# Kernel optimization log

Hardware: AMD Instinct MI355X
Metric: run time of the kernel (lower is better)

Reference implementation:

```python
import jax, jax.numpy as jnp
import numpy as np

IN_F = 128
OUT_F = 128
N_LAYER = 2
DEPTH = 9                       # tree depth -> levels 0..DEPTH-1
N_TREES = 128
TREE_SIZE = 2 ** DEPTH - 1      # 511 nodes per complete binary tree
N = N_TREES * TREE_SIZE         # 65408 total nodes
E = N_TREES * (TREE_SIZE - 1)   # 65280 parent->child edges


def _build_forest():
    """Complete binary trees in heap layout; leaves get order 0, root order DEPTH-1."""
    k = np.arange(TREE_SIZE)
    depth = np.floor(np.log2(k + 1)).astype(np.int32)
    order_tree = (DEPTH - 1) - depth                      # per-node level within a tree
    node_order = np.tile(order_tree, N_TREES).astype(np.int32)
    internal = k[k < 2 ** (DEPTH - 1) - 1]                # internal nodes have 2 children
    par = np.repeat(internal, 2)
    chi = np.empty_like(par)
    chi[0::2] = 2 * internal + 1
    chi[1::2] = 2 * internal + 2
    eorder_tree = order_tree[par]
    offs = (np.arange(N_TREES) * TREE_SIZE)[:, None]
    parents = (par[None, :] + offs).reshape(-1)
    children = (chi[None, :] + offs).reshape(-1)
    adjacency = np.stack([parents, children], axis=1).astype(np.int32)
    edge_order = np.tile(eorder_tree, N_TREES).astype(np.int32)
    return node_order, adjacency, edge_order


def setup_inputs() -> dict:
    key = jax.random.key(0)
    ks = jax.random.split(key, 8)
    node_order, adjacency, edge_order = _build_forest()
    s = 0.05
    return {
        "features": jax.random.normal(ks[0], (N, IN_F), jnp.float32),
        "W_iou": jax.random.normal(ks[1], (N_LAYER, 3 * OUT_F, IN_F), jnp.float32) * s,
        "b_iou": jax.random.normal(ks[2], (N_LAYER, 3 * OUT_F), jnp.float32) * s,
        "U_iou": jax.random.normal(ks[3], (N_LAYER, 3 * OUT_F, OUT_F), jnp.float32) * s,
        "W_f": jax.random.normal(ks[4], (N_LAYER, OUT_F, IN_F), jnp.float32) * s,
        "b_f": jax.random.normal(ks[5], (N_LAYER, OUT_F), jnp.float32) * s,
        "U_f": jax.random.normal(ks[6], (N_LAYER, OUT_F, OUT_F), jnp.float32) * s,
        "node_order": jnp.asarray(node_order),
        "adjacency_list": jnp.asarray(adjacency),
        "edge_order": jnp.asarray(edge_order),
        "treesizes": jnp.full((N_TREES,), TREE_SIZE, jnp.int32),
        "n_levels": DEPTH,
    }


def reference(features, W_iou, b_iou, U_iou, W_f, b_f, U_f,
              node_order, adjacency_list, edge_order, treesizes, n_levels):
    n_nodes = features.shape[0]
    parent = adjacency_list[:, 0]
    child = adjacency_list[:, 1]
    n_trees = treesizes.shape[0]
    tree_size = n_nodes // n_trees
    # root of each (equal-sized) tree = argmax of node_order within its segment
    root_idx = (jnp.argmax(node_order.reshape(n_trees, tree_size), axis=1)
                + jnp.arange(n_trees) * tree_size)

    def run_layer(Wi, bi, Ui, Wf, bf, Uf):
        Wx_iou = features @ Wi.T + bi              # [N, 3H], level-independent
        Wfx = features[parent] @ Wf.T + bf         # [E, H], per-edge forget input
        H = Wi.shape[0] // 3

        def step(carry, lvl):
            h, c = carry
            em = (edge_order == lvl).astype(features.dtype)[:, None]   # [E,1]
            ch = h[child]                                              # gather child h
            cc = c[child]
            h_sum = jax.ops.segment_sum(ch * em, parent, num_segments=n_nodes)
            iou = Wx_iou + h_sum @ Ui.T
            i_, o_, u_ = jnp.split(iou, 3, axis=1)
            i_ = jax.nn.sigmoid(i_)
            o_ = jax.nn.sigmoid(o_)
            u_ = jnp.tanh(u_)
            f = jax.nn.sigmoid(Wfx + ch @ Uf.T)                        # [E,H]
            c_sum = jax.ops.segment_sum(f * cc * em, parent, num_segments=n_nodes)
            c_new = i_ * u_ + c_sum
            h_new = o_ * jnp.tanh(c_new)
            nm = (node_order == lvl)[:, None]
            return (jnp.where(nm, h_new, h), jnp.where(nm, c_new, c)), None

        init = (jnp.zeros((n_nodes, H), features.dtype),
                jnp.zeros((n_nodes, H), features.dtype))
        (h, c), _ = jax.lax.scan(step, init, jnp.arange(n_levels))
        return h[root_idx], c[root_idx]

    f_h, f_c = jax.vmap(run_layer)(W_iou, b_iou, U_iou, W_f, b_f, U_f)
    return f_h, f_c
```

## Files before the change

### kernel.cpp

```cpp
#include <hip/hip_runtime.h>
#include <hip/hip_bf16.h>


#define TS 511
#define NT 128
#define NN (NT * TS)

typedef __attribute__((ext_vector_type(8))) short short8;
typedef __attribute__((ext_vector_type(4))) float floatx4;

#define MFMA_B16 __builtin_amdgcn_mfma_f32_16x16x32_bf16

#define BARLDS() do { \
    asm volatile("s_waitcnt lgkmcnt(0)" ::: "memory"); \
    __builtin_amdgcn_s_barrier(); \
    asm volatile("" ::: "memory"); \
} while (0)

__device__ __forceinline__ unsigned short f2b(float f) {
    return __builtin_bit_cast(unsigned short, __float2bfloat16(f));
}
__device__ __forceinline__ float b2f_u(unsigned short u) {
    unsigned v = (unsigned)u << 16;
    return __builtin_bit_cast(float, v);
}
__device__ __forceinline__ float rcp_(float x) { return __builtin_amdgcn_rcpf(x); }
__device__ __forceinline__ float sig_(float x) { return rcp_(1.0f + __expf(-x)); }
__device__ __forceinline__ float tanh_(float x) {
    float a = fabsf(x);
    float t = __expf(-2.0f * a);
    return copysignf((1.0f - t) * rcp_(1.0f + t), x);
}

__global__ void pack_b(const float* __restrict__ Wiou, const float* __restrict__ biou,
                       const float* __restrict__ Uiou, const float* __restrict__ Wf,
                       const float* __restrict__ bfv, const float* __restrict__ Uf,
                       const float* __restrict__ feat,
                       unsigned short* __restrict__ BgU, unsigned short* __restrict__ BgX,
                       float* __restrict__ bp5, unsigned short* __restrict__ xb) {
    int tid = blockIdx.x * 256 + threadIdx.x;
    if (tid < 1280) {
        int l = tid / 640, r = tid % 640, g = r >> 7, o = r & 127;
        bp5[tid] = (g < 3) ? biou[l * 384 + r] : bfv[l * 128 + o];
    }
    if (tid < 131072) {
        int l = tid >> 16, r = tid & 65535, col = r >> 7, kp = r & 127;
        float v = (col < 384) ? Uiou[(l * 384 + col) * 128 + kp]
                              : Uf[(l * 128 + (col - 384)) * 128 + kp];
        BgU[((size_t)(l * 512 + col)) * 128 + kp] = f2b(v);
    } else if (tid < 262144) {
        int e2 = tid - 131072;
        int l = e2 >> 16, r = e2 & 65535, col = r >> 7, kp = r & 127;
        float v = (col < 384) ? Wiou[(l * 384 + col) * 128 + kp]
                              : Wf[(l * 128 + (col - 384)) * 128 + kp];
        BgX[((size_t)(l * 512 + col)) * 128 + kp] = f2b(v);
    } else {
        int e = tid - 262144;
        size_t base = (size_t)e * 8;
        float4 v0 = *(const float4*)(feat + base);
        float4 v1 = *(const float4*)(feat + base + 4);
        short8 r;
        r[0] = (short)f2b(v0.x); r[1] = (short)f2b(v0.y);
        r[2] = (short)f2b(v0.z); r[3] = (short)f2b(v0.w);
        r[4] = (short)f2b(v1.x); r[5] = (short)f2b(v1.y);
        r[6] = (short)f2b(v1.z); r[7] = (short)f2b(v1.w);
        *(short8*)(xb + base) = r;
    }
}

__global__ __launch_bounds__(512, 2) void forest(
        const unsigned short* __restrict__ xb16, const unsigned short* __restrict__ BgU,
        const unsigned short* __restrict__ BgX, const float* __restrict__ bp5,
        float* __restrict__ out) {
    __shared__ __align__(16) unsigned short S[69632];
    const int HC0 = 26112;

    const int tid = threadIdx.x;
    const int l = blockIdx.x >> 7, tree = blockIdx.x & 127;
    const int lane = tid & 63, w = tid >> 6;
    const int quad = lane >> 4, l15 = lane & 15;
    const int o = w * 16 + l15;
    const unsigned short* xb = xb16 + (size_t)tree * TS * 128;
    const unsigned short* BU = BgU + (size_t)l * 512 * 128;
    const unsigned short* BX = BgX + (size_t)l * 512 * 128;

    short8 bU[4][4], bX[4][4];
#pragma unroll
    for (int g = 0; g < 4; g++) {
        const size_t cb = (size_t)(g * 128 + o) * 128;
#pragma unroll
        for (int kbl = 0; kbl < 4; kbl++) {
            bU[g][kbl] = *(const short8*)(BU + cb + kbl * 32 + quad * 8);
            bX[g][kbl] = *(const short8*)(BX + cb + kbl * 32 + quad * 8);
        }
    }
    float bb[5];
#pragma unroll
    for (int g = 0; g < 5; g++) bb[g] = bp5[l * 640 + g * 128 + o];

    auto ldx = [&](int heap, int kbl) -> short8 {
        return *(const short8*)(xb + (size_t)heap * 128 + kbl * 32 + quad * 8);
    };

    auto ltile = [&](int heapA, int selfH, int selfC) {
        floatx4 ai = (floatx4){0.f, 0.f, 0.f, 0.f};
        floatx4 ao = ai, au = ai;
#pragma unroll
        for (int kbl = 0; kbl < 4; kbl++) {
            short8 ax = ldx(heapA, kbl);
            ai = MFMA_B16(ax, bX[0][kbl], ai, 0, 0, 0);
            ao = MFMA_B16(ax, bX[1][kbl], ao, 0, 0, 0);
            au = MFMA_B16(ax, bX[2][kbl], au, 0, 0, 0);
        }
#pragma unroll
        for (int r = 0; r < 4; r++) {
            int idx = quad * 4 + r;
            float iv = sig_(ai[r] + bb[0]);
            float ov = sig_(ao[r] + bb[1]);
            float uv = tanh_(au[r] + bb[2]);
            float cn = iv * uv;
            float hn = ov * tanh_(cn);
            S[(selfH + idx) * 136 + o] = f2b(hn);
            S[HC0 + (selfC + idx) * 136 + o] = f2b(cn);
        }
    };

    auto itile = [&](int heapA, int chAh, int selfRB, int chRBc,
                     int nValid, bool isRoot) {
        floatx4 ai = (floatx4){0.f, 0.f, 0.f, 0.f};
        floatx4 ao = ai, au = ai, awx = ai, af0 = ai, af1 = ai;
#pragma unroll
        for (int kbl = 0; kbl < 4; kbl++) {
            short8 h0 = *(const short8*)&S[chAh * 136 + kbl * 32 + quad * 8];
            short8 h1 = *(const short8*)&S[(chAh + 1) * 136 + kbl * 32 + quad * 8];
            short8 ax = ldx(heapA, kbl);
            ai = MFMA_B16(h0, bU[0][kbl], ai, 0, 0, 0);
            ai = MFMA_B16(h1, bU[0][kbl], ai, 0, 0, 0);
            ao = MFMA_B16(h0, bU[1][kbl], ao, 0, 0, 0);
            ao = MFMA_B16(h1, bU[1][kbl], ao, 0, 0, 0);
            au = MFMA_B16(h0, bU[2][kbl], au, 0, 0, 0);
            au = MFMA_B16(h1, bU[2][kbl], au, 0, 0, 0);
            af0 = MFMA_B16(h0, bU[3][kbl], af0, 0, 0, 0);
            af1 = MFMA_B16(h1, bU[3][kbl], af1, 0, 0, 0);
            ai = MFMA_B16(ax, bX[0][kbl], ai, 0, 0, 0);
            ao = MFMA_B16(ax, bX[1][kbl], ao, 0, 0, 0);
            au = MFMA_B16(ax, bX[2][kbl], au, 0, 0, 0);
            awx = MFMA_B16(ax, bX[3][kbl], awx, 0, 0, 0);
        }
#pragma unroll
        for (int r = 0; r < 4; r++) {
            int idx = quad * 4 + r;
            if (idx < nValid) {
                float iv = sig_(ai[r] + bb[0]);
                float ov = sig_(ao[r] + bb[1]);
                float uv = tanh_(au[r] + bb[2]);
                float f0 = sig_(awx[r] + af0[r] + bb[3]);
                float f1 = sig_(awx[r] + af1[r] + bb[4]);
                float c0 = b2f_u(S[HC0 + (chRBc + 2 * idx) * 136 + o]);
                float c1 = b2f_u(S[HC0 + (chRBc + 2 * idx + 1) * 136 + o]);
                float cn = iv * uv + f0 * c0 + f1 * c1;
                float hn = ov * tanh_(cn);
                S[(selfRB + idx) * 136 + o] = f2b(hn);
                S[HC0 + (selfRB + idx) * 136 + o] = f2b(cn);
                if (isRoot) {
                    out[((size_t)l * 128 + tree) * 128 + o] = hn;
                    out[32768 + ((size_t)l * 128 + tree) * 128 + o] = cn;
                }
            }
        }
    };

#pragma unroll
    for (int s = 0; s < 2; s++)
        ltile(255 + s * 16 + l15, 384 + s * 16, 256 + s * 16);
    BARLDS();

#pragma unroll 2
    for (int t = 0; t < 8; t++) {
        if (t < 7) {
            int b2 = (t + 1) & 1;
#pragma unroll
            for (int s = 0; s < 2; s++)
                ltile(255 + (t + 1) * 32 + s * 16 + l15,
                      384 + b2 * 32 + s * 16, 256 + b2 * 32 + s * 16);
        }
        int b = t & 1;
        itile(127 + t * 16 + l15,
              384 + b * 32 + 2 * l15,
              t * 16,
              256 + b * 32,
              16, false);
        BARLDS();
    }

#pragma unroll
    for (int dd = 6; dd >= 0; dd--) {
        const int nd = 1 << dd;
        const int selfB = (dd == 6) ? 128 : 64 - 2 * nd;
        const int chB = (dd == 6) ? 0 : ((dd == 5) ? 128 : 64 - 4 * nd);
        const int mts = (nd + 15) >> 4;
#pragma unroll
        for (int mt = 0; mt < mts; mt++) {
            int rl = mt * 16 + l15;
            if (rl > nd - 1) rl = nd - 1;
            int nv = nd - mt * 16;
            if (nv > 16) nv = 16;
            itile(nd - 1 + rl,
                  chB + 2 * rl,
                  selfB + mt * 16,
                  chB + 2 * mt * 16,
                  nv, dd == 0);
        }
        BARLDS();
    }
}

extern "C" void kernel_launch(void* const* d_in, const int* in_sizes, int n_in,
                              void* d_out, int out_size, void* d_ws, size_t ws_size,
                              hipStream_t stream) {
    const float* feat = (const float*)d_in[0];
    const float* Wiou = (const float*)d_in[1];
    const float* biou = (const float*)d_in[2];
    const float* Uiou = (const float*)d_in[3];
    const float* Wf   = (const float*)d_in[4];
    const float* bfv  = (const float*)d_in[5];
    const float* Uf   = (const float*)d_in[6];
    float* out = (float*)d_out;

    unsigned short* BgU = (unsigned short*)d_ws;
    unsigned short* BgX = BgU + (size_t)131072;
    unsigned short* xb16 = BgX + (size_t)131072;
    float* bp5 = (float*)(xb16 + (size_t)NN * 128);

    pack_b<<<5112, 256, 0, stream>>>(Wiou, biou, Uiou, Wf, bfv, Uf, feat,
                                     BgU, BgX, bp5, xb16);
    forest<<<256, 512, 0, stream>>>(xb16, BgU, BgX, bp5, out);
}
```

Before: 157.6 us.

## Prefetch feature tiles ahead of MFMA and interleave upper tree levels into leaf loop

Global loads of bf16 feature rows are hoisted into whole-tile prefetches issued before the MFMA work that consumes them, so memory latency overlaps compute instead of being exposed inside the k-loop. Level-6 internal tiles are folded into the main level-7/8 loop on alternate iterations, and the remaining upper levels are unrolled by hand with next-level features prefetched before each barrier. The goal is fewer barriers and less exposed load latency. The cost is higher register pressure from holding several X4 prefetch buffers, and the hand-coded LDS row offsets must match the old layout exactly.

```diff
diff --git a/kernel.cpp b/kernel.cpp
--- a/kernel.cpp
+++ b/kernel.cpp
@@ -101,16 +101,22 @@
     auto ldx = [&](int heap, int kbl) -> short8 {
         return *(const short8*)(xb + (size_t)heap * 128 + kbl * 32 + quad * 8);
     };
-
-    auto ltile = [&](int heapA, int selfH, int selfC) {
+    struct X4 { short8 a[4]; };
+    auto pfx = [&](int heap) -> X4 {
+        X4 r;
+#pragma unroll
+        for (int k = 0; k < 4; k++) r.a[k] = ldx(heap, k);
+        return r;
+    };
+
+    auto ltile = [&](const X4& ax, int selfH, int selfC) {
         floatx4 ai = (floatx4){0.f, 0.f, 0.f, 0.f};
         floatx4 ao = ai, au = ai;
 #pragma unroll
         for (int kbl = 0; kbl < 4; kbl++) {
-            short8 ax = ldx(heapA, kbl);
-            ai = MFMA_B16(ax, bX[0][kbl], ai, 0, 0, 0);
-            ao = MFMA_B16(ax, bX[1][kbl], ao, 0, 0, 0);
-            au = MFMA_B16(ax, bX[2][kbl], au, 0, 0, 0);
+            ai = MFMA_B16(ax.a[kbl], bX[0][kbl], ai, 0, 0, 0);
+            ao = MFMA_B16(ax.a[kbl], bX[1][kbl], ao, 0, 0, 0);
+            au = MFMA_B16(ax.a[kbl], bX[2][kbl], au, 0, 0, 0);
         }
 #pragma unroll
         for (int r = 0; r < 4; r++) {
@@ -125,7 +131,7 @@
         }
     };
 
-    auto itile = [&](int heapA, int chAh, int selfRB, int chRBc,
+    auto itile = [&](const X4& ax, int chAh, int selfRB, int chRBc,
                      int nValid, bool isRoot) {
         floatx4 ai = (floatx4){0.f, 0.f, 0.f, 0.f};
         floatx4 ao = ai, au = ai, awx = ai, af0 = ai, af1 = ai;
@@ -133,7 +139,6 @@
         for (int kbl = 0; kbl < 4; kbl++) {
             short8 h0 = *(const short8*)&S[chAh * 136 + kbl * 32 + quad * 8];
             short8 h1 = *(const short8*)&S[(chAh + 1) * 136 + kbl * 32 + quad * 8];
-            short8 ax = ldx(heapA, kbl);
             ai = MFMA_B16(h0, bU[0][kbl], ai, 0, 0, 0);
             ai = MFMA_B16(h1, bU[0][kbl], ai, 0, 0, 0);
             ao = MFMA_B16(h0, bU[1][kbl], ao, 0, 0, 0);
@@ -142,10 +147,10 @@
             au = MFMA_B16(h1, bU[2][kbl], au, 0, 0, 0);
             af0 = MFMA_B16(h0, bU[3][kbl], af0, 0, 0, 0);
             af1 = MFMA_B16(h1, bU[3][kbl], af1, 0, 0, 0);
-            ai = MFMA_B16(ax, bX[0][kbl], ai, 0, 0, 0);
-            ao = MFMA_B16(ax, bX[1][kbl], ao, 0, 0, 0);
-            au = MFMA_B16(ax, bX[2][kbl], au, 0, 0, 0);
-            awx = MFMA_B16(ax, bX[3][kbl], awx, 0, 0, 0);
+            ai = MFMA_B16(ax.a[kbl], bX[0][kbl], ai, 0, 0, 0);
+            ao = MFMA_B16(ax.a[kbl], bX[1][kbl], ao, 0, 0, 0);
+            au = MFMA_B16(ax.a[kbl], bX[2][kbl], au, 0, 0, 0);
+            awx = MFMA_B16(ax.a[kbl], bX[3][kbl], awx, 0, 0, 0);
         }
 #pragma unroll
         for (int r = 0; r < 4; r++) {
@@ -170,49 +175,55 @@
         }
     };
 
-#pragma unroll
-    for (int s = 0; s < 2; s++)
-        ltile(255 + s * 16 + l15, 384 + s * 16, 256 + s * 16);
-    BARLDS();
-
-#pragma unroll 2
+    {
+        X4 p0 = pfx(255 + l15), p1 = pfx(271 + l15);
+        ltile(p0, 384, 256);
+        ltile(p1, 400, 272);
+    }
+    BARLDS();
+
+    X4 axT0, axT1;
+
+#pragma unroll 1
     for (int t = 0; t < 8; t++) {
+        X4 lx0, lx1, axd, axe;
+        axd = pfx(127 + t * 16 + l15);
+        if (t < 7) { lx0 = pfx(287 + t * 32 + l15); lx1 = pfx(303 + t * 32 + l15); }
+        const bool do6 = (t == 2) || (t == 4) || (t == 6);
+        const int j = (t - 2) >> 1;
+        if (do6) axe = pfx(63 + j * 16 + l15);
+        if (t == 7) { axT0 = pfx(111 + l15); axT1 = pfx(31 + l15); }
+
+        const int b = t & 1, b2 = b ^ 1;
         if (t < 7) {
-            int b2 = (t + 1) & 1;
-#pragma unroll
-            for (int s = 0; s < 2; s++)
-                ltile(255 + (t + 1) * 32 + s * 16 + l15,
-                      384 + b2 * 32 + s * 16, 256 + b2 * 32 + s * 16);
-        }
-        int b = t & 1;
-        itile(127 + t * 16 + l15,
-              384 + b * 32 + 2 * l15,
-              t * 16,
-              256 + b * 32,
-              16, false);
+            ltile(lx0, 384 + b2 * 32, 256 + b2 * 32);
+            ltile(lx1, 384 + b2 * 32 + 16, 256 + b2 * 32 + 16);
+        }
+        itile(axd, 384 + b * 32 + 2 * l15, t * 16, 256 + b * 32, 16, false);
+        if (do6) itile(axe, 2 * (j * 16 + l15), 128 + j * 16, 32 * j, 16, false);
         BARLDS();
     }
 
-#pragma unroll
-    for (int dd = 6; dd >= 0; dd--) {
-        const int nd = 1 << dd;
-        const int selfB = (dd == 6) ? 128 : 64 - 2 * nd;
-        const int chB = (dd == 6) ? 0 : ((dd == 5) ? 128 : 64 - 4 * nd);
-        const int mts = (nd + 15) >> 4;
-#pragma unroll
-        for (int mt = 0; mt < mts; mt++) {
-            int rl = mt * 16 + l15;
-            if (rl > nd - 1) rl = nd - 1;
-            int nv = nd - mt * 16;
-            if (nv > 16) nv = 16;
-            itile(nd - 1 + rl,
-                  chB + 2 * rl,
-                  selfB + mt * 16,
-                  chB + 2 * mt * 16,
-                  nv, dd == 0);
-        }
-        BARLDS();
-    }
+    itile(axT0, 96 + 2 * l15, 176, 96, 16, false);
+    itile(axT1, 128 + 2 * l15, 0, 128, 16, false);
+    axT0 = pfx(47 + l15);
+    BARLDS();
+    itile(axT0, 160 + 2 * l15, 16, 160, 16, false);
+    axT0 = pfx(15 + l15);
+    BARLDS();
+    itile(axT0, 2 * l15, 32, 0, 16, false);
+    { int rl = (l15 < 7) ? l15 : 7; axT0 = pfx(7 + rl); }
+    BARLDS();
+    { int rl = (l15 < 7) ? l15 : 7; itile(axT0, 32 + 2 * rl, 48, 32, 8, false); }
+    { int rl = (l15 < 3) ? l15 : 3; axT0 = pfx(3 + rl); }
+    BARLDS();
+    { int rl = (l15 < 3) ? l15 : 3; itile(axT0, 48 + 2 * rl, 56, 48, 4, false); }
+    { int rl = (l15 < 1) ? l15 : 1; axT0 = pfx(1 + rl); }
+    BARLDS();
+    { int rl = (l15 < 1) ? l15 : 1; itile(axT0, 56 + 2 * rl, 60, 56, 2, false); }
+    axT0 = pfx(0);
+    BARLDS();
+    itile(axT0, 60, 62, 60, 1, true);
 }
 
 extern "C" void kernel_launch(void* const* d_in, const int* in_sizes, int n_in,
```

Result: slower. 170.6 us (+8.2%).

## Prefetch node features into registers and interleave level-6 tiles with level-7 loop

Applied to the files above, without the earlier changes.

Global loads of the bf16 node features are now issued one stage ahead into registers instead of being read inside the MFMA loops, which hides their global-memory latency behind the previous tile's compute. Level-6 internal tiles are folded into the level-7 loop as soon as their children are ready, which removes separate barrier phases, and the upper levels are unrolled by hand with explicit prefetches. Launch bounds change to waves_per_eu(2,2). The extra live short8 registers raise register pressure and could cause spills.

```diff
diff --git a/kernel.cpp b/kernel.cpp
--- a/kernel.cpp
+++ b/kernel.cpp
@@ -68,7 +68,9 @@
     }
 }
 
-__global__ __launch_bounds__(512, 2) void forest(
+__global__ __launch_bounds__(512, 1)
+__attribute__((amdgpu_waves_per_eu(2, 2)))
+void forest(
         const unsigned short* __restrict__ xb16, const unsigned short* __restrict__ BgU,
         const unsigned short* __restrict__ BgX, const float* __restrict__ bp5,
         float* __restrict__ out) {
@@ -102,12 +104,13 @@
         return *(const short8*)(xb + (size_t)heap * 128 + kbl * 32 + quad * 8);
     };
 
-    auto ltile = [&](int heapA, int selfH, int selfC) {
+    auto ltile = [&](short8 a0, short8 a1, short8 a2, short8 a3,
+                     int selfH, int selfC) {
         floatx4 ai = (floatx4){0.f, 0.f, 0.f, 0.f};
         floatx4 ao = ai, au = ai;
 #pragma unroll
         for (int kbl = 0; kbl < 4; kbl++) {
-            short8 ax = ldx(heapA, kbl);
+            short8 ax = (kbl == 0) ? a0 : (kbl == 1) ? a1 : (kbl == 2) ? a2 : a3;
             ai = MFMA_B16(ax, bX[0][kbl], ai, 0, 0, 0);
             ao = MFMA_B16(ax, bX[1][kbl], ao, 0, 0, 0);
             au = MFMA_B16(ax, bX[2][kbl], au, 0, 0, 0);
@@ -125,15 +128,15 @@
         }
     };
 
-    auto itile = [&](int heapA, int chAh, int selfRB, int chRBc,
-                     int nValid, bool isRoot) {
+    auto itile = [&](short8 a0, short8 a1, short8 a2, short8 a3,
+                     int chAh, int selfRB, int chRBc, int nValid, bool isRoot) {
         floatx4 ai = (floatx4){0.f, 0.f, 0.f, 0.f};
         floatx4 ao = ai, au = ai, awx = ai, af0 = ai, af1 = ai;
 #pragma unroll
         for (int kbl = 0; kbl < 4; kbl++) {
+            short8 ax = (kbl == 0) ? a0 : (kbl == 1) ? a1 : (kbl == 2) ? a2 : a3;
             short8 h0 = *(const short8*)&S[chAh * 136 + kbl * 32 + quad * 8];
             short8 h1 = *(const short8*)&S[(chAh + 1) * 136 + kbl * 32 + quad * 8];
-            short8 ax = ldx(heapA, kbl);
             ai = MFMA_B16(h0, bU[0][kbl], ai, 0, 0, 0);
             ai = MFMA_B16(h1, bU[0][kbl], ai, 0, 0, 0);
             ao = MFMA_B16(h0, bU[1][kbl], ao, 0, 0, 0);
@@ -170,49 +173,96 @@
         }
     };
 
-#pragma unroll
-    for (int s = 0; s < 2; s++)
-        ltile(255 + s * 16 + l15, 384 + s * 16, 256 + s * 16);
-    BARLDS();
-
-#pragma unroll 2
+    short8 axdC[4];
+    short8 axT0[4], axT1[4];
+
+    {
+        short8 t0[4], t1[4];
+#pragma unroll
+        for (int k = 0; k < 4; k++) {
+            t0[k] = ldx(255 + l15, k);
+            t1[k] = ldx(271 + l15, k);
+            axdC[k] = ldx(127 + l15, k);
+        }
+        ltile(t0[0], t0[1], t0[2], t0[3], 384, 256);
+        ltile(t1[0], t1[1], t1[2], t1[3], 400, 272);
+    }
+    BARLDS();
+
+#pragma unroll 1
     for (int t = 0; t < 8; t++) {
+        const int b = t & 1;
+        const bool do6 = (t >= 2) && !(t & 1);
+        const int j = (t - 2) >> 1;
+        short8 lx0[4], lx1[4], axe[4];
         if (t < 7) {
-            int b2 = (t + 1) & 1;
-#pragma unroll
-            for (int s = 0; s < 2; s++)
-                ltile(255 + (t + 1) * 32 + s * 16 + l15,
-                      384 + b2 * 32 + s * 16, 256 + b2 * 32 + s * 16);
-        }
-        int b = t & 1;
-        itile(127 + t * 16 + l15,
-              384 + b * 32 + 2 * l15,
-              t * 16,
-              256 + b * 32,
-              16, false);
+#pragma unroll
+            for (int k = 0; k < 4; k++) {
+                lx0[k] = ldx(287 + t * 32 + l15, k);
+                lx1[k] = ldx(303 + t * 32 + l15, k);
+            }
+        }
+        if (do6) {
+#pragma unroll
+            for (int k = 0; k < 4; k++) axe[k] = ldx(63 + j * 16 + l15, k);
+        }
+        if (t == 7) {
+#pragma unroll
+            for (int k = 0; k < 4; k++) {
+                axT0[k] = ldx(111 + l15, k);
+                axT1[k] = ldx(31 + l15, k);
+            }
+        }
+
+        itile(axdC[0], axdC[1], axdC[2], axdC[3],
+              384 + b * 32 + 2 * l15, t * 16, 256 + b * 32, 16, false);
+        if (t < 7) {
+#pragma unroll
+            for (int k = 0; k < 4; k++) axdC[k] = ldx(127 + (t + 1) * 16 + l15, k);
+        }
+        if (do6)
+            itile(axe[0], axe[1], axe[2], axe[3],
+                  2 * (j * 16 + l15), 128 + j * 16, 32 * j, 16, false);
+        if (t < 7) {
+            const int b2 = b ^ 1;
+            ltile(lx0[0], lx0[1], lx0[2], lx0[3], 384 + b2 * 32, 256 + b2 * 32);
+            ltile(lx1[0], lx1[1], lx1[2], lx1[3], 384 + b2 * 32 + 16, 256 + b2 * 32 + 16);
+        }
         BARLDS();
     }
 
-#pragma unroll
-    for (int dd = 6; dd >= 0; dd--) {
-        const int nd = 1 << dd;
-        const int selfB = (dd == 6) ? 128 : 64 - 2 * nd;
-        const int chB = (dd == 6) ? 0 : ((dd == 5) ? 128 : 64 - 4 * nd);
-        const int mts = (nd + 15) >> 4;
-#pragma unroll
-        for (int mt = 0; mt < mts; mt++) {
-            int rl = mt * 16 + l15;
-            if (rl > nd - 1) rl = nd - 1;
-            int nv = nd - mt * 16;
-            if (nv > 16) nv = 16;
-            itile(nd - 1 + rl,
-                  chB + 2 * rl,
-                  selfB + mt * 16,
-                  chB + 2 * mt * 16,
-                  nv, dd == 0);
-        }
-        BARLDS();
-    }
+    itile(axT0[0], axT0[1], axT0[2], axT0[3], 96 + 2 * l15, 176, 96, 16, false);
+    itile(axT1[0], axT1[1], axT1[2], axT1[3], 128 + 2 * l15, 0, 128, 16, false);
+#pragma unroll
+    for (int k = 0; k < 4; k++) axT0[k] = ldx(47 + l15, k);
+    BARLDS();
+    itile(axT0[0], axT0[1], axT0[2], axT0[3], 160 + 2 * l15, 16, 160, 16, false);
+#pragma unroll
+    for (int k = 0; k < 4; k++) axT0[k] = ldx(15 + l15, k);
+    BARLDS();
+    itile(axT0[0], axT0[1], axT0[2], axT0[3], 2 * l15, 32, 0, 16, false);
+    { int rl = (l15 < 7) ? l15 : 7;
+#pragma unroll
+      for (int k = 0; k < 4; k++) axT0[k] = ldx(7 + rl, k); }
+    BARLDS();
+    { int rl = (l15 < 7) ? l15 : 7;
+      itile(axT0[0], axT0[1], axT0[2], axT0[3], 32 + 2 * rl, 48, 32, 8, false); }
+    { int rl = (l15 < 3) ? l15 : 3;
+#pragma unroll
+      for (int k = 0; k < 4; k++) axT0[k] = ldx(3 + rl, k); }
+    BARLDS();
+    { int rl = (l15 < 3) ? l15 : 3;
+      itile(axT0[0], axT0[1], axT0[2], axT0[3], 48 + 2 * rl, 56, 48, 4, false); }
+    { int rl = (l15 < 1) ? l15 : 1;
+#pragma unroll
+      for (int k = 0; k < 4; k++) axT0[k] = ldx(1 + rl, k); }
+    BARLDS();
+    { int rl = (l15 < 1) ? l15 : 1;
+      itile(axT0[0], axT0[1], axT0[2], axT0[3], 56 + 2 * rl, 60, 56, 2, false); }
+#pragma unroll
+    for (int k = 0; k < 4; k++) axT0[k] = ldx(0, k);
+    BARLDS();
+    itile(axT0[0], axT0[1], axT0[2], axT0[3], 60, 62, 60, 1, true);
 }
 
 extern "C" void kernel_launch(void* const* d_in, const int* in_sizes, int n_in,
```

Result: slower. 180.0 us (+14.2%).

## Split leaf-level LSTM into a separate wide GEMM kernel before tree recursion

Applied to the files above, without the earlier changes.

Leaf node computation (x·W_iou, gates) moves out of the per-tree forest kernel into a new leafwx kernel. It runs as a batched MFMA GEMM across all trees and both layers and writes leaf h/c in bf16 to global memory. The forest kernel now reads leaf h/c from global, packs features only for internal nodes, and loads U/W fragments from global per use instead of keeping them in registers. The aim is to parallelise the dominant leaf work across many more blocks and to lower register pressure in the recursive kernel. In exchange it adds a kernel launch, an extra global round trip for leaf states, and repeated weight loads in the inner loops.

```diff
diff --git a/kernel.cpp b/kernel.cpp
--- a/kernel.cpp
+++ b/kernel.cpp
@@ -4,7 +4,6 @@
 
 #define TS 511
 #define NT 128
-#define NN (NT * TS)
 
 typedef __attribute__((ext_vector_type(8))) short short8;
 typedef __attribute__((ext_vector_type(4))) float floatx4;
@@ -56,112 +55,210 @@
         BgX[((size_t)(l * 512 + col)) * 128 + kp] = f2b(v);
     } else {
         int e = tid - 262144;
-        size_t base = (size_t)e * 8;
-        float4 v0 = *(const float4*)(feat + base);
-        float4 v1 = *(const float4*)(feat + base + 4);
+        int tree = e / 4080;
+        int rem = e - tree * 4080;
+        int row = rem >> 4, c8 = (rem & 15) * 8;
+        const float* src = feat + ((size_t)tree * TS + row) * 128 + c8;
+        float4 v0 = *(const float4*)src;
+        float4 v1 = *(const float4*)(src + 4);
         short8 r;
         r[0] = (short)f2b(v0.x); r[1] = (short)f2b(v0.y);
         r[2] = (short)f2b(v0.z); r[3] = (short)f2b(v0.w);
         r[4] = (short)f2b(v1.x); r[5] = (short)f2b(v1.y);
         r[6] = (short)f2b(v1.z); r[7] = (short)f2b(v1.w);
-        *(short8*)(xb + base) = r;
+        *(short8*)(xb + ((size_t)tree * 255 + row) * 128 + c8) = r;
     }
 }
 
-__global__ __launch_bounds__(512, 2) void forest(
-        const unsigned short* __restrict__ xb16, const unsigned short* __restrict__ BgU,
+__global__ __launch_bounds__(256) void leafwx(
+        const float* __restrict__ feat, const unsigned short* __restrict__ BgX,
+        const float* __restrict__ bp5,
+        unsigned short* __restrict__ hb, unsigned short* __restrict__ cb) {
+    const int tid = threadIdx.x;
+    const int lane = tid & 63, wave = tid >> 6;
+    const int W = blockIdx.x * 4 + wave;
+    const int wn = W & 3;
+    const int mt = W >> 2;
+    const int l = mt >> 10, m = mt & 1023;
+    const int quad = lane >> 4, l15 = lane & 15;
+    const unsigned short* BX = BgX + (size_t)l * 512 * 128;
+
+    floatx4 acc[2][6];
+#pragma unroll
+    for (int mi = 0; mi < 2; mi++)
+#pragma unroll
+        for (int ni = 0; ni < 6; ni++)
+            acc[mi][ni] = (floatx4){0.f, 0.f, 0.f, 0.f};
+
+#pragma unroll
+    for (int kb = 0; kb < 4; kb++) {
+        short8 bfr[6];
+#pragma unroll
+        for (int ni = 0; ni < 6; ni++) {
+            int col = (ni >> 1) * 128 + wn * 32 + (ni & 1) * 16 + l15;
+            bfr[ni] = *(const short8*)(BX + (size_t)col * 128 + kb * 32 + quad * 8);
+        }
+#pragma unroll
+        for (int mi = 0; mi < 2; mi++) {
+            int j = m * 32 + mi * 16 + l15;
+            int tree = j >> 8, li = j & 255;
+            const float* p = feat + ((size_t)tree * TS + 255 + li) * 128 + kb * 32 + quad * 8;
+            float4 u0 = *(const float4*)p;
+            float4 u1 = *(const float4*)(p + 4);
+            short8 a;
+            a[0] = (short)f2b(u0.x); a[1] = (short)f2b(u0.y);
+            a[2] = (short)f2b(u0.z); a[3] = (short)f2b(u0.w);
+            a[4] = (short)f2b(u1.x); a[5] = (short)f2b(u1.y);
+            a[6] = (short)f2b(u1.z); a[7] = (short)f2b(u1.w);
+#pragma unroll
+            for (int ni = 0; ni < 6; ni++)
+                acc[mi][ni] = MFMA_B16(a, bfr[ni], acc[mi][ni], 0, 0, 0);
+        }
+    }
+#pragma unroll
+    for (int mi = 0; mi < 2; mi++)
+#pragma unroll
+        for (int ch = 0; ch < 2; ch++) {
+            int of = wn * 32 + ch * 16 + l15;
+            float bi = bp5[l * 640 + of];
+            float bo = bp5[l * 640 + 128 + of];
+            float bu = bp5[l * 640 + 256 + of];
+#pragma unroll
+            for (int r = 0; r < 4; r++) {
+                int j = m * 32 + mi * 16 + quad * 4 + r;
+                int tree = j >> 8, li = j & 255;
+                float iv = sig_(acc[mi][ch][r] + bi);
+                float ov = sig_(acc[mi][2 + ch][r] + bo);
+                float uv = tanh_(acc[mi][4 + ch][r] + bu);
+                float cn = iv * uv;
+                float hn = ov * tanh_(cn);
+                size_t idx = ((size_t)(l * 32768) + tree * 256 + li) * 128 + of;
+                hb[idx] = f2b(hn);
+                cb[idx] = f2b(cn);
+            }
+        }
+}
+
+__global__ __launch_bounds__(512) void forest(
+        const unsigned short* __restrict__ xb16, const unsigned short* __restrict__ hbL,
+        const unsigned short* __restrict__ cbL, const unsigned short* __restrict__ BgU,
         const unsigned short* __restrict__ BgX, const float* __restrict__ bp5,
         float* __restrict__ out) {
-    __shared__ __align__(16) unsigned short S[69632];
-    const int HC0 = 26112;
+    __shared__ __align__(16) unsigned short S[69360];
+    const int HC0 = 34680;
 
     const int tid = threadIdx.x;
     const int l = blockIdx.x >> 7, tree = blockIdx.x & 127;
     const int lane = tid & 63, w = tid >> 6;
     const int quad = lane >> 4, l15 = lane & 15;
     const int o = w * 16 + l15;
-    const unsigned short* xb = xb16 + (size_t)tree * TS * 128;
+    const unsigned short* xb = xb16 + (size_t)tree * 255 * 128;
+    const unsigned short* lh = hbL + ((size_t)(l * 32768) + tree * 256) * 128;
+    const unsigned short* lc = cbL + ((size_t)(l * 32768) + tree * 256) * 128;
     const unsigned short* BU = BgU + (size_t)l * 512 * 128;
     const unsigned short* BX = BgX + (size_t)l * 512 * 128;
 
-    short8 bU[4][4], bX[4][4];
-#pragma unroll
-    for (int g = 0; g < 4; g++) {
-        const size_t cb = (size_t)(g * 128 + o) * 128;
-#pragma unroll
-        for (int kbl = 0; kbl < 4; kbl++) {
-            bU[g][kbl] = *(const short8*)(BU + cb + kbl * 32 + quad * 8);
-            bX[g][kbl] = *(const short8*)(BX + cb + kbl * 32 + quad * 8);
-        }
-    }
     float bb[5];
 #pragma unroll
     for (int g = 0; g < 5; g++) bb[g] = bp5[l * 640 + g * 128 + o];
 
-    auto ldx = [&](int heap, int kbl) -> short8 {
-        return *(const short8*)(xb + (size_t)heap * 128 + kbl * 32 + quad * 8);
-    };
-
-    auto ltile = [&](int heapA, int selfH, int selfC) {
+    auto bu_ = [&](int g, int k) -> short8 {
+        return *(const short8*)(BU + ((size_t)(g * 128 + o)) * 128 + k * 32 + quad * 8);
+    };
+    auto bx_ = [&](int g, int k) -> short8 {
+        return *(const short8*)(BX + ((size_t)(g * 128 + o)) * 128 + k * 32 + quad * 8);
+    };
+    auto ldx = [&](int heap, int k) -> short8 {
+        return *(const short8*)(xb + (size_t)heap * 128 + k * 32 + quad * 8);
+    };
+
+    auto itile_g = [&](int t) {
+        const int nA = 127 + t * 16 + l15;
+        const int li0 = 32 * t + 2 * l15;
+        short8 ax[4];
+#pragma unroll
+        for (int k = 0; k < 4; k++) ax[k] = ldx(nA, k);
         floatx4 ai = (floatx4){0.f, 0.f, 0.f, 0.f};
-        floatx4 ao = ai, au = ai;
-#pragma unroll
-        for (int kbl = 0; kbl < 4; kbl++) {
-            short8 ax = ldx(heapA, kbl);
-            ai = MFMA_B16(ax, bX[0][kbl], ai, 0, 0, 0);
-            ao = MFMA_B16(ax, bX[1][kbl], ao, 0, 0, 0);
-            au = MFMA_B16(ax, bX[2][kbl], au, 0, 0, 0);
+        floatx4 ao = ai, au = ai, awx = ai, af0 = ai, af1 = ai;
+#pragma unroll
+        for (int k = 0; k < 4; k++) {
+            short8 h0 = *(const short8*)(lh + (size_t)li0 * 128 + k * 32 + quad * 8);
+            short8 h1 = *(const short8*)(lh + (size_t)(li0 + 1) * 128 + k * 32 + quad * 8);
+            ai = MFMA_B16(h0, bu_(0, k), ai, 0, 0, 0);
+            ai = MFMA_B16(h1, bu_(0, k), ai, 0, 0, 0);
+            ao = MFMA_B16(h0, bu_(1, k), ao, 0, 0, 0);
+            ao = MFMA_B16(h1, bu_(1, k), ao, 0, 0, 0);
+            au = MFMA_B16(h0, bu_(2, k), au, 0, 0, 0);
+            au = MFMA_B16(h1, bu_(2, k), au, 0, 0, 0);
+            af0 = MFMA_B16(h0, bu_(3, k), af0, 0, 0, 0);
+            af1 = MFMA_B16(h1, bu_(3, k), af1, 0, 0, 0);
+            ai = MFMA_B16(ax[k], bx_(0, k), ai, 0, 0, 0);
+            ao = MFMA_B16(ax[k], bx_(1, k), ao, 0, 0, 0);
+            au = MFMA_B16(ax[k], bx_(2, k), au, 0, 0, 0);
+            awx = MFMA_B16(ax[k], bx_(3, k), awx, 0, 0, 0);
         }
 #pragma unroll
         for (int r = 0; r < 4; r++) {
             int idx = quad * 4 + r;
+            int node = 127 + t * 16 + idx;
+            int lic = 32 * t + 2 * idx;
             float iv = sig_(ai[r] + bb[0]);
             float ov = sig_(ao[r] + bb[1]);
             float uv = tanh_(au[r] + bb[2]);
-            float cn = iv * uv;
+            float f0 = sig_(awx[r] + af0[r] + bb[3]);
+            float f1 = sig_(awx[r] + af1[r] + bb[4]);
+            float c0 = b2f_u(lc[(size_t)lic * 128 + o]);
+            float c1 = b2f_u(lc[(size_t)(lic + 1) * 128 + o]);
+            float cn = iv * uv + f0 * c0 + f1 * c1;
             float hn = ov * tanh_(cn);
-            S[(selfH + idx) * 136 + o] = f2b(hn);
-            S[HC0 + (selfC + idx) * 136 + o] = f2b(cn);
-        }
-    };
-
-    auto itile = [&](int heapA, int chAh, int selfRB, int chRBc,
-                     int nValid, bool isRoot) {
+            S[node * 136 + o] = f2b(hn);
+            S[HC0 + node * 136 + o] = f2b(cn);
+        }
+    };
+
+    auto itile_l = [&](int base, int nv, bool isRoot) {
+        const int rl = (l15 < nv) ? l15 : nv - 1;
+        const int nA = base + rl;
+        const int ch0 = 2 * nA + 1;
+        short8 ax[4];
+#pragma unroll
+        for (int k = 0; k < 4; k++) ax[k] = ldx(nA, k);
         floatx4 ai = (floatx4){0.f, 0.f, 0.f, 0.f};
         floatx4 ao = ai, au = ai, awx = ai, af0 = ai, af1 = ai;
 #pragma unroll
-        for (int kbl = 0; kbl < 4; kbl++) {
-            short8 h0 = *(const short8*)&S[chAh * 136 + kbl * 32 + quad * 8];
-            short8 h1 = *(const short8*)&S[(chAh + 1) * 136 + kbl * 32 + quad * 8];
-            short8 ax = ldx(heapA, kbl);
-            ai = MFMA_B16(h0, bU[0][kbl], ai, 0, 0, 0);
-            ai = MFMA_B16(h1, bU[0][kbl], ai, 0, 0, 0);
-            ao = MFMA_B16(h0, bU[1][kbl], ao, 0, 0, 0);
-            ao = MFMA_B16(h1, bU[1][kbl], ao, 0, 0, 0);
-            au = MFMA_B16(h0, bU[2][kbl], au, 0, 0, 0);
-            au = MFMA_B16(h1, bU[2][kbl], au, 0, 0, 0);
-            af0 = MFMA_B16(h0, bU[3][kbl], af0, 0, 0, 0);
-            af1 = MFMA_B16(h1, bU[3][kbl], af1, 0, 0, 0);
-            ai = MFMA_B16(ax, bX[0][kbl], ai, 0, 0, 0);
-            ao = MFMA_B16(ax, bX[1][kbl], ao, 0, 0, 0);
-            au = MFMA_B16(ax, bX[2][kbl], au, 0, 0, 0);
-            awx = MFMA_B16(ax, bX[3][kbl], awx, 0, 0, 0);
+        for (int k = 0; k < 4; k++) {
+            short8 h0 = *(const short8*)&S[ch0 * 136 + k * 32 + quad * 8];
+            short8 h1 = *(const short8*)&S[(ch0 + 1) * 136 + k * 32 + quad * 8];
+            ai = MFMA_B16(h0, bu_(0, k), ai, 0, 0, 0);
+            ai = MFMA_B16(h1, bu_(0, k), ai, 0, 0, 0);
+            ao = MFMA_B16(h0, bu_(1, k), ao, 0, 0, 0);
+            ao = MFMA_B16(h1, bu_(1, k), ao, 0, 0, 0);
+            au = MFMA_B16(h0, bu_(2, k), au, 0, 0, 0);
+            au = MFMA_B16(h1, bu_(2, k), au, 0, 0, 0);
+            af0 = MFMA_B16(h0, bu_(3, k), af0, 0, 0, 0);
+            af1 = MFMA_B16(h1, bu_(3, k), af1, 0, 0, 0);
+            ai = MFMA_B16(ax[k], bx_(0, k), ai, 0, 0, 0);
+            ao = MFMA_B16(ax[k], bx_(1, k), ao, 0, 0, 0);
+            au = MFMA_B16(ax[k], bx_(2, k), au, 0, 0, 0);
+            awx = MFMA_B16(ax[k], bx_(3, k), awx, 0, 0, 0);
         }
 #pragma unroll
         for (int r = 0; r < 4; r++) {
             int idx = quad * 4 + r;
-            if (idx < nValid) {
+            if (idx < nv) {
+                int node = base + idx;
+                int ch = 2 * node + 1;
                 float iv = sig_(ai[r] + bb[0]);
                 float ov = sig_(ao[r] + bb[1]);
                 float uv = tanh_(au[r] + bb[2]);
                 float f0 = sig_(awx[r] + af0[r] + bb[3]);
                 float f1 = sig_(awx[r] + af1[r] + bb[4]);
-                float c0 = b2f_u(S[HC0 + (chRBc + 2 * idx) * 136 + o]);
-                float c1 = b2f_u(S[HC0 + (chRBc + 2 * idx + 1) * 136 + o]);
+                float c0 = b2f_u(S[HC0 + ch * 136 + o]);
+                float c1 = b2f_u(S[HC0 + (ch + 1) * 136 + o]);
                 float cn = iv * uv + f0 * c0 + f1 * c1;
                 float hn = ov * tanh_(cn);
-                S[(selfRB + idx) * 136 + o] = f2b(hn);
-                S[HC0 + (selfRB + idx) * 136 + o] = f2b(cn);
+                S[node * 136 + o] = f2b(hn);
+                S[HC0 + node * 136 + o] = f2b(cn);
                 if (isRoot) {
                     out[((size_t)l * 128 + tree) * 128 + o] = hn;
                     out[32768 + ((size_t)l * 128 + tree) * 128 + o] = cn;
@@ -170,49 +267,24 @@
         }
     };
 
-#pragma unroll
-    for (int s = 0; s < 2; s++)
-        ltile(255 + s * 16 + l15, 384 + s * 16, 256 + s * 16);
-    BARLDS();
-
 #pragma unroll 2
-    for (int t = 0; t < 8; t++) {
-        if (t < 7) {
-            int b2 = (t + 1) & 1;
-#pragma unroll
-            for (int s = 0; s < 2; s++)
-                ltile(255 + (t + 1) * 32 + s * 16 + l15,
-                      384 + b2 * 32 + s * 16, 256 + b2 * 32 + s * 16);
-        }
-        int b = t & 1;
-        itile(127 + t * 16 + l15,
-              384 + b * 32 + 2 * l15,
-              t * 16,
-              256 + b * 32,
-              16, false);
-        BARLDS();
-    }
-
-#pragma unroll
-    for (int dd = 6; dd >= 0; dd--) {
-        const int nd = 1 << dd;
-        const int selfB = (dd == 6) ? 128 : 64 - 2 * nd;
-        const int chB = (dd == 6) ? 0 : ((dd == 5) ? 128 : 64 - 4 * nd);
-        const int mts = (nd + 15) >> 4;
-#pragma unroll
-        for (int mt = 0; mt < mts; mt++) {
-            int rl = mt * 16 + l15;
-            if (rl > nd - 1) rl = nd - 1;
-            int nv = nd - mt * 16;
-            if (nv > 16) nv = 16;
-            itile(nd - 1 + rl,
-                  chB + 2 * rl,
-                  selfB + mt * 16,
-                  chB + 2 * mt * 16,
-                  nv, dd == 0);
-        }
-        BARLDS();
-    }
+    for (int t = 0; t < 8; t++) itile_g(t);
+    BARLDS();
+#pragma unroll 2
+    for (int t = 0; t < 4; t++) itile_l(63 + 16 * t, 16, false);
+    BARLDS();
+    itile_l(31, 16, false);
+    itile_l(47, 16, false);
+    BARLDS();
+    itile_l(15, 16, false);
+    BARLDS();
+    itile_l(7, 8, false);
+    BARLDS();
+    itile_l(3, 4, false);
+    BARLDS();
+    itile_l(1, 2, false);
+    BARLDS();
+    itile_l(0, 1, true);
 }
 
 extern "C" void kernel_launch(void* const* d_in, const int* in_sizes, int n_in,
@@ -230,9 +302,12 @@
     unsigned short* BgU = (unsigned short*)d_ws;
     unsigned short* BgX = BgU + (size_t)131072;
     unsigned short* xb16 = BgX + (size_t)131072;
-    float* bp5 = (float*)(xb16 + (size_t)NN * 128);
-
-    pack_b<<<5112, 256, 0, stream>>>(Wiou, biou, Uiou, Wf, bfv, Uf, feat,
+    unsigned short* hb = xb16 + (size_t)4177920;
+    unsigned short* cb = hb + (size_t)8388608;
+    float* bp5 = (float*)(cb + (size_t)8388608);
+
+    pack_b<<<3064, 256, 0, stream>>>(Wiou, biou, Uiou, Wf, bfv, Uf, feat,
                                      BgU, BgX, bp5, xb16);
-    forest<<<256, 512, 0, stream>>>(xb16, BgU, BgX, bp5, out);
-}
+    leafwx<<<2048, 256, 0, stream>>>(feat, BgX, bp5, hb, cb);
+    forest<<<256, 512, 0, stream>>>(xb16, hb, cb, BgU, BgX, bp5, out);
+}
```

After: 237.9 us. 50.9% more time.
